# Kernel tuning notes

Hardware: AMD Instinct MI355X
Metric: run time of the kernel (lower is better)

Reference implementation:

```python
import jax, jax.numpy as jnp
import numpy as np

B, A, T, D, H, ATTN = 32, 128, 96, 16, 128, 64
MAX_DIST, EMB = 50, 32


def _ln(x, g, b, eps=1e-5):
    m = x.mean(-1, keepdims=True)
    v = ((x - m) ** 2).mean(-1, keepdims=True)
    return (x - m) / jnp.sqrt(v + eps) * g + b


def _lstm_layer(xs, Wih, Whh, bih, bhh):
    # xs: (N, T, Din); PyTorch gate order i, f, g, o
    n = xs.shape[0]
    h0 = jnp.zeros((n, Whh.shape[1]), xs.dtype)
    bias = bih + bhh
    def step(carry, x_t):
        h, c = carry
        gates = x_t @ Wih.T + h @ Whh.T + bias
        i, f, g, o = jnp.split(gates, 4, axis=-1)
        c = jax.nn.sigmoid(f) * c + jax.nn.sigmoid(i) * jnp.tanh(g)
        h = jax.nn.sigmoid(o) * jnp.tanh(c)
        return (h, c), h
    _, hs = jax.lax.scan(step, (h0, h0), jnp.swapaxes(xs, 0, 1))
    return jnp.swapaxes(hs, 0, 1)  # (N, T, H)


def _forward(ranks, x, W_ih0, W_hh0, b_ih0, b_hh0, W_ih1, W_hh1, b_ih1, b_hh1,
             attn_w, attn_W1, attn_W2, ln1_g, ln1_b, proj_W, proj_b,
             Wq, bq, Wk, bk, Wv, bv, rank_emb, rw1_W, rw1_b, rw2_W,
             ff1_W, ff1_b, ff2_W, ff2_b, ln2_g, ln2_b, sp1_W, sp1_b, sp2_W, sp2_b):
    b, a, t, d = x.shape
    xs = x.reshape(b * a, t, d)
    # LSTM-HA (dropout disabled, eval mode)
    h1 = _lstm_layer(xs, W_ih0, W_hh0, b_ih0, b_hh0)
    h2 = _lstm_layer(h1, W_ih1, W_hh1, b_ih1, b_hh1)
    hT = h2[:, -1, :]
    # additive history attention, vectorized over all timesteps
    alpha = jnp.tanh(h2 @ attn_W1 + (hT @ attn_W2)[:, None, :]) @ attn_w  # (b*a, t)
    w = jax.nn.softmax(alpha, axis=1)
    ctx = jnp.einsum('nt,nth->nh', w, h2)
    rep = _ln(ctx, ln1_g, ln1_b).reshape(b, a, -1)  # (b, a, H)
    # CAAN
    xp = rep @ proj_W + proj_b
    q = xp @ Wq + bq
    k = xp @ Wk + bk
    v = xp @ Wv + bv
    scores = jnp.einsum('bnd,bmd->bnm', q, k) / (ATTN ** 0.5)
    dist = jnp.clip(jnp.abs(ranks[:, :, None] - ranks[:, None, :]), 0, MAX_DIST)
    emb = rank_emb[dist]  # (b, a, a, EMB)
    gate = jax.nn.sigmoid(jax.nn.relu(emb @ rw1_W + rw1_b) @ rw2_W)  # (b, a, a)
    attn = jax.nn.softmax(scores * gate, axis=-1)
    ao = jnp.einsum('bnm,bmd->bnd', attn, v)
    ff = _ln(jax.nn.relu(ao @ ff1_W + ff1_b) @ ff2_W + ff2_b, ln2_g, ln2_b)
    return jax.nn.sigmoid((jax.nn.relu(ff @ sp1_W + sp1_b) @ sp2_W + sp2_b)[..., 0])


def setup_inputs() -> dict:
    key = jax.random.key(0)
    ks = jax.random.split(key, 40)
    it = iter(range(40))
    def rn(shape, s):
        return jax.random.normal(ks[next(it)], shape, jnp.float32) * s
    sH = 1.0 / float(np.sqrt(H))
    sA = 1.0 / float(np.sqrt(ATTN))
    return dict(
        x=jax.random.normal(ks[next(it)], (B, A, T, D), jnp.float32),
        ranks=jax.random.randint(ks[next(it)], (B, A), 0, A),
        W_ih0=rn((4 * H, D), sH), W_hh0=rn((4 * H, H), sH),
        b_ih0=jnp.zeros(4 * H), b_hh0=jnp.zeros(4 * H),
        W_ih1=rn((4 * H, H), sH), W_hh1=rn((4 * H, H), sH),
        b_ih1=jnp.zeros(4 * H), b_hh1=jnp.zeros(4 * H),
        attn_w=rn((H,), 0.06), attn_W1=rn((H, H), sH), attn_W2=rn((H, H), sH),
        ln1_g=jnp.ones(H), ln1_b=jnp.zeros(H),
        proj_W=rn((H, ATTN), sH), proj_b=jnp.zeros(ATTN),
        Wq=rn((ATTN, ATTN), sA), bq=jnp.zeros(ATTN),
        Wk=rn((ATTN, ATTN), sA), bk=jnp.zeros(ATTN),
        Wv=rn((ATTN, ATTN), sA), bv=jnp.zeros(ATTN),
        rank_emb=rn((MAX_DIST + 1, EMB), 1.0),
        rw1_W=rn((EMB, 16), 1.0 / float(np.sqrt(EMB))), rw1_b=jnp.zeros(16),
        rw2_W=rn((16,), 0.25),
        ff1_W=rn((ATTN, 2 * ATTN), sA), ff1_b=jnp.zeros(2 * ATTN),
        ff2_W=rn((2 * ATTN, ATTN), 1.0 / float(np.sqrt(2 * ATTN))), ff2_b=jnp.zeros(ATTN),
        ln2_g=jnp.ones(ATTN), ln2_b=jnp.zeros(ATTN),
        sp1_W=rn((ATTN, 32), sA), sp1_b=jnp.zeros(32),
        sp2_W=rn((32, 1), 0.18), sp2_b=jnp.zeros(1),
    )


def reference(x, ranks, W_ih0, W_hh0, b_ih0, b_hh0, W_ih1, W_hh1, b_ih1, b_hh1,
              attn_w, attn_W1, attn_W2, ln1_g, ln1_b, proj_W, proj_b,
              Wq, bq, Wk, bk, Wv, bv, rank_emb, rw1_W, rw1_b, rw2_W,
              ff1_W, ff1_b, ff2_W, ff2_b, ln2_g, ln2_b, sp1_W, sp1_b, sp2_W, sp2_b):
    return _forward(ranks, x, W_ih0, W_hh0, b_ih0, b_hh0, W_ih1, W_hh1, b_ih1, b_hh1,
                    attn_w, attn_W1, attn_W2, ln1_g, ln1_b, proj_W, proj_b,
                    Wq, bq, Wk, bk, Wv, bv, rank_emb, rw1_W, rw1_b, rw2_W,
                    ff1_W, ff1_b, ff2_W, ff2_b, ln2_g, ln2_b, sp1_W, sp1_b, sp2_W, sp2_b)
```

## Files before the change

### kernel.cpp

```cpp
#include <hip/hip_runtime.h>
#include <hip/hip_bf16.h>

namespace {

constexpr int T_ = 96;
constexpr int H_ = 128;

typedef short s8v __attribute__((ext_vector_type(8)));
typedef float f4v __attribute__((ext_vector_type(4)));

__device__ __forceinline__ float rcp_(float x) { return __builtin_amdgcn_rcpf(x); }
__device__ __forceinline__ float sig_(float x) { return rcp_(1.f + __expf(-x)); }
__device__ __forceinline__ float tanh_(float x) { return 1.f - 2.f * rcp_(__expf(2.f * x) + 1.f); }

__device__ __forceinline__ unsigned short bf16u(float f) {
  union { float f; unsigned u; } v; v.f = f;
  unsigned r = v.u + 0x7FFFu + ((v.u >> 16) & 1u);
  return (unsigned short)(r >> 16);
}
__device__ __forceinline__ float bf2f(unsigned short b) {
  union { unsigned u; float f; } v; v.u = ((unsigned)b) << 16;
  return v.f;
}

__device__ __forceinline__ s8v load8(const float* __restrict__ p) {
  const float4 a = *reinterpret_cast<const float4*>(p);
  const float4 b = *reinterpret_cast<const float4*>(p + 4);
  s8v r;
  r[0] = (short)bf16u(a.x); r[1] = (short)bf16u(a.y);
  r[2] = (short)bf16u(a.z); r[3] = (short)bf16u(a.w);
  r[4] = (short)bf16u(b.x); r[5] = (short)bf16u(b.y);
  r[6] = (short)bf16u(b.z); r[7] = (short)bf16u(b.w);
  return r;
}

__device__ __forceinline__ f4v mfma16(s8v a, s8v b, f4v c) {
  return __builtin_amdgcn_mfma_f32_16x16x32_bf16(a, b, c, 0, 0, 0);
}

__device__ __forceinline__ void barrier_lds() {
  __builtin_amdgcn_sched_barrier(0);
  asm volatile("s_waitcnt lgkmcnt(0)" ::: "memory");
  __builtin_amdgcn_s_barrier();
  __builtin_amdgcn_sched_barrier(0);
}

__global__ __launch_bounds__(64) void k0_gate(
    const float* __restrict__ remb,
    const float* __restrict__ rw1W, const float* __restrict__ rw1b,
    const float* __restrict__ rw2W,
    float* __restrict__ glut)
{
  const int d = threadIdx.x;
  if (d > 50) return;
  const float* er = remb + d * 32;
  float g = 0.f;
#pragma unroll
  for (int e = 0; e < 16; ++e) {
    float hs = rw1b[e];
#pragma unroll 8
    for (int i = 0; i < 32; ++i) hs += er[i] * rw1W[i * 16 + e];
    g += fmaxf(hs, 0.f) * rw2W[e];
  }
  glut[d] = sig_(g);
}

__global__ __launch_bounds__(256) void k0_w1(
    const float* __restrict__ W1, unsigned short* __restrict__ w1f)
{
  const int e = blockIdx.x * 256 + threadIdx.x;
  const int k = e >> 7, nn = e & 127;
  const int f = ((((nn >> 4) * 4 + (k >> 5)) * 4 + ((k >> 3) & 3)) * 16 + (nn & 15)) * 8 + (k & 7);
  w1f[f] = bf16u(W1[e]);
}

__global__ __launch_bounds__(256) void k0_whh1(
    const float* __restrict__ Whh1, unsigned short* __restrict__ whh1f)
{
  const int e = blockIdx.x * 256 + threadIdx.x;
  const int n = e >> 7, k = e & 127;
  const int g = n >> 7, wl = (n >> 4) & 7, l16 = n & 15;
  const int kt = k >> 5, lq = (k >> 3) & 3, i = k & 7;
  const int dst = (((g * 8 + wl) * 4 + kt) * 64 + lq * 16 + l16) * 8 + i;
  whh1f[dst] = bf16u(Whh1[e]);
}

__global__ __launch_bounds__(512) void k1_lstm_mfma(
    const float* __restrict__ x,
    const float* __restrict__ Wih0, const float* __restrict__ Whh0,
    const float* __restrict__ bih0, const float* __restrict__ bhh0,
    const float* __restrict__ Wih1, const float* __restrict__ whh1f,
    const float* __restrict__ bih1, const float* __restrict__ bhh1,
    unsigned short* __restrict__ hist)
{
  __shared__ __align__(16) unsigned short w1l[512 * 128];
  __shared__ __align__(16) unsigned short h1s[2][16 * 128];
  __shared__ __align__(16) unsigned short h2s[2][16 * 128];
  __shared__ __align__(16) unsigned short xb[2][16 * 32];

  const int tid  = threadIdx.x;
  const int lane = tid & 63;
  const int wv   = tid >> 6;
  const int l16  = lane & 15;
  const int lq   = lane >> 4;
  const int seqbase = blockIdx.x * 16;

  for (int i = tid; i < 2 * 16 * 128; i += 512) {
    (&h1s[0][0])[i] = 0; (&h2s[0][0])[i] = 0;
  }
  if (tid < 256) {
    const int s = tid >> 4, d = tid & 15;
    xb[0][s * 32 + 16 + d] = 0; xb[1][s * 32 + 16 + d] = 0;
    xb[0][s * 32 + d] = bf16u(x[((size_t)(seqbase + s) * T_ + 0) * 16 + d]);
  }
  {
    const uint4* src = reinterpret_cast<const uint4*>(whh1f);
    uint4* dst = reinterpret_cast<uint4*>(w1l);
    for (int i = tid; i < 8192; i += 512) dst[i] = src[i];
  }

  s8v whh0[4][4], wih1[4][4], wx0[4];
  float b0[4], b1[4];
  int wb[4];
#pragma unroll
  for (int g = 0; g < 4; ++g) {
    const int gr = g * 128 + 16 * wv + l16;
    b0[g] = bih0[gr] + bhh0[gr];
    b1[g] = bih1[gr] + bhh1[gr];
    wb[g] = ((g * 8 + wv) * 4) * 1024 + lane * 16;
#pragma unroll
    for (int kt = 0; kt < 4; ++kt) {
      const int k0 = kt * 32 + lq * 8;
      whh0[g][kt] = load8(Whh0 + (size_t)gr * 128 + k0);
      wih1[g][kt] = load8(Wih1 + (size_t)gr * 128 + k0);
    }
    if (lq < 2) wx0[g] = load8(Wih0 + (size_t)gr * 16 + lq * 8);
    else { s8v z; for (int i2 = 0; i2 < 8; ++i2) z[i2] = 0; wx0[g] = z; }
  }

  float c1[4] = {0.f, 0.f, 0.f, 0.f}, c2[4] = {0.f, 0.f, 0.f, 0.f};
  int cur = 0;
  __syncthreads();

  const int sw = (l16 & 7) << 4;
  const int hunit = 16 * wv + l16;

  for (int t = 0; t < T_; ++t) {
    const int xc = t & 1;
    float xv = 0.f;
    const bool xpf = (t + 1 < T_) && (tid < 256);
    if (xpf) {
      const int s = tid >> 4, d = tid & 15;
      xv = x[((size_t)(seqbase + s) * T_ + (t + 1)) * 16 + d];
    }

    f4v acc[4];
#pragma unroll
    for (int g = 0; g < 4; ++g) acc[g] = f4v{b0[g], b0[g], b0[g], b0[g]};
    {
      const s8v ax = *reinterpret_cast<const s8v*>(
          reinterpret_cast<const char*>(&xb[xc][0]) + l16 * 64 + lq * 16);
#pragma unroll
      for (int g = 0; g < 4; ++g) acc[g] = mfma16(ax, wx0[g], acc[g]);
    }
#pragma unroll
    for (int kt = 0; kt < 4; ++kt) {
      const s8v ah = *reinterpret_cast<const s8v*>(
          reinterpret_cast<const char*>(&h1s[cur][0]) + l16 * 256 +
          ((kt * 64 + lq * 16) ^ sw));
#pragma unroll
      for (int g = 0; g < 4; ++g) acc[g] = mfma16(ah, whh0[g][kt], acc[g]);
    }
#pragma unroll
    for (int ss = 0; ss < 4; ++ss) {
      const int seq = lq * 4 + ss;
      const float iv = sig_(acc[0][ss]);
      const float fv = sig_(acc[1][ss]);
      const float gv = tanh_(acc[2][ss]);
      const float ov = sig_(acc[3][ss]);
      c1[ss] = fv * c1[ss] + iv * gv;
      const float hv = ov * tanh_(c1[ss]);
      *reinterpret_cast<unsigned short*>(
          reinterpret_cast<char*>(&h1s[cur ^ 1][0]) + seq * 256 +
          ((2 * hunit) ^ ((seq & 7) << 4))) = bf16u(hv);
    }
    barrier_lds();

#pragma unroll
    for (int g = 0; g < 4; ++g) acc[g] = f4v{b1[g], b1[g], b1[g], b1[g]};
#pragma unroll
    for (int kt = 0; kt < 4; ++kt) {
      const int ko = (kt * 64 + lq * 16) ^ sw;
      const s8v a1 = *reinterpret_cast<const s8v*>(
          reinterpret_cast<const char*>(&h1s[cur ^ 1][0]) + l16 * 256 + ko);
      const s8v a2 = *reinterpret_cast<const s8v*>(
          reinterpret_cast<const char*>(&h2s[cur][0]) + l16 * 256 + ko);
#pragma unroll
      for (int g = 0; g < 4; ++g) {
        acc[g] = mfma16(a1, wih1[g][kt], acc[g]);
        const s8v bw = *reinterpret_cast<const s8v*>(
            reinterpret_cast<const char*>(w1l) + wb[g] + kt * 1024);
        acc[g] = mfma16(a2, bw, acc[g]);
      }
    }
#pragma unroll
    for (int ss = 0; ss < 4; ++ss) {
      const int seq = lq * 4 + ss;
      const float iv = sig_(acc[0][ss]);
      const float fv = sig_(acc[1][ss]);
      const float gv = tanh_(acc[2][ss]);
      const float ov = sig_(acc[3][ss]);
      c2[ss] = fv * c2[ss] + iv * gv;
      const float hv = ov * tanh_(c2[ss]);
      *reinterpret_cast<unsigned short*>(
          reinterpret_cast<char*>(&h2s[cur ^ 1][0]) + seq * 256 +
          ((2 * hunit) ^ ((seq & 7) << 4))) = bf16u(hv);
    }
    if (xpf) {
      const int s = tid >> 4, d = tid & 15;
      xb[xc ^ 1][s * 32 + d] = bf16u(xv);
    }
    barrier_lds();

    {
      const int seq = tid >> 5;
      const int u0  = (tid & 31) * 4;
      const uint2 v = *reinterpret_cast<const uint2*>(
          reinterpret_cast<const char*>(&h2s[cur ^ 1][0]) + seq * 256 +
          ((2 * u0) ^ ((seq & 7) << 4)));
      *reinterpret_cast<uint2*>(
          hist + ((size_t)(seqbase + seq) * T_ + t) * H_ + u0) = v;
    }
    cur ^= 1;
  }
}

__global__ __launch_bounds__(384, 2) void k2_pool_mfma(
    const unsigned short* __restrict__ hist,
    const unsigned short* __restrict__ w1f,
    const float* __restrict__ attn_w,
    const float* __restrict__ W2,
    const float* __restrict__ ln1g, const float* __restrict__ ln1b,
    float* __restrict__ rep)
{
  __shared__ __align__(16) unsigned short hst[96 * 128];
  __shared__ float sS[128], aws[128], alpha[96], wts[96], red[128], hTs[128];
  __shared__ float ctxP[3][128];

  const int n = blockIdx.x;
  const int tid = threadIdx.x;
  const int lane = tid & 63;
  const int wv = tid >> 6;
  const int l16 = lane & 15;
  const int lq = lane >> 4;

  const unsigned short* hsrc = hist + (size_t)n * T_ * H_;
  for (int i = tid; i < 1536; i += 384) {
    const int row = i >> 4, c16 = i & 15;
    const uint4 v = *reinterpret_cast<const uint4*>(hsrc + row * 128 + c16 * 8);
    *reinterpret_cast<uint4*>(
        reinterpret_cast<char*>(hst) + row * 256 + ((c16 * 16) ^ ((row & 7) << 4))) = v;
  }
  if (tid < 128) aws[tid] = attn_w[tid];
  __syncthreads();

  if (tid < 128) hTs[tid] = bf2f(hst[95 * 128 + (tid ^ 56)]);
  __syncthreads();
  if (tid < 128) {
    float s = 0.f;
    for (int h = 0; h < 128; ++h) s += hTs[h] * W2[(size_t)h * 128 + tid];
    sS[tid] = s;
  }
  __syncthreads();

  {
    const int row0 = wv * 16 + l16;
    f4v acc[8];
#pragma unroll
    for (int nt = 0; nt < 8; ++nt) acc[nt] = f4v{0.f, 0.f, 0.f, 0.f};
#pragma unroll
    for (int kt = 0; kt < 4; ++kt) {
      const s8v a = *reinterpret_cast<const s8v*>(
          reinterpret_cast<const char*>(hst) + row0 * 256 +
          ((kt * 64 + lq * 16) ^ ((row0 & 7) << 4)));
#pragma unroll
      for (int nt = 0; nt < 8; ++nt) {
        const s8v b = *reinterpret_cast<const s8v*>(
            w1f + ((((nt << 2) + kt) << 2 | lq) * 16 + l16) * 8);
        acc[nt] = mfma16(a, b, acc[nt]);
      }
    }
    float pa[4] = {0.f, 0.f, 0.f, 0.f};
#pragma unroll
    for (int nt = 0; nt < 8; ++nt) {
      const int col = nt * 16 + l16;
      const float ss = sS[col], aw = aws[col];
#pragma unroll
      for (int i2 = 0; i2 < 4; ++i2) pa[i2] += tanh_(acc[nt][i2] + ss) * aw;
    }
#pragma unroll
    for (int i2 = 0; i2 < 4; ++i2) {
      float v = pa[i2];
      v += __shfl_xor(v, 8); v += __shfl_xor(v, 4);
      v += __shfl_xor(v, 2); v += __shfl_xor(v, 1);
      if (l16 == 0) alpha[wv * 16 + lq * 4 + i2] = v;
    }
  }
  __syncthreads();

  if (tid < 128) red[tid] = (tid < 96) ? alpha[tid] : -1e30f;
  __syncthreads();
  for (int sft = 64; sft > 0; sft >>= 1) {
    if (tid < sft) red[tid] = fmaxf(red[tid], red[tid + sft]);
    __syncthreads();
  }
  const float mx = red[0];
  __syncthreads();
  if (tid < 128) {
    const float e = (tid < 96) ? __expf(alpha[tid] - mx) : 0.f;
    red[tid] = e;
    if (tid < 96) wts[tid] = e;
  }
  __syncthreads();
  for (int sft = 64; sft > 0; sft >>= 1) {
    if (tid < sft) red[tid] += red[tid + sft];
    __syncthreads();
  }
  const float inv = rcp_(red[0]);
  if (tid < 96) wts[tid] *= inv;
  __syncthreads();

  {
    const int th = tid >> 7, j = tid & 127;
    float cp = 0.f;
    for (int t = th * 32; t < th * 32 + 32; ++t)
      cp += wts[t] * bf2f(hst[t * 128 + (j ^ ((t & 7) << 3))]);
    ctxP[th][j] = cp;
  }
  __syncthreads();
  if (tid < 128) {
    hTs[tid] = ctxP[0][tid] + ctxP[1][tid] + ctxP[2][tid];
    red[tid] = hTs[tid];
  }
  __syncthreads();
  for (int sft = 64; sft > 0; sft >>= 1) {
    if (tid < sft) red[tid] += red[tid + sft];
    __syncthreads();
  }
  const float mean = red[0] * (1.f / 128.f);
  __syncthreads();
  if (tid < 128) { const float d = hTs[tid] - mean; red[tid] = d * d; }
  __syncthreads();
  for (int sft = 64; sft > 0; sft >>= 1) {
    if (tid < sft) red[tid] += red[tid + sft];
    __syncthreads();
  }
  const float var = red[0] * (1.f / 128.f);
  if (tid < 128)
    rep[(size_t)n * H_ + tid] =
        (hTs[tid] - mean) * rsqrtf(var + 1e-5f) * ln1g[tid] + ln1b[tid];
}

__global__ __launch_bounds__(256) void k3_qkv(
    const float* __restrict__ rep,
    const float* __restrict__ projW, const float* __restrict__ projb,
    const float* __restrict__ Wq, const float* __restrict__ bq,
    const float* __restrict__ Wk, const float* __restrict__ bk,
    const float* __restrict__ Wv, const float* __restrict__ bv,
    float* __restrict__ q, float* __restrict__ k, float* __restrict__ v)
{
  const int rbase = blockIdx.x * 32;
  const int tid = threadIdx.x;
  __shared__ float reps[32][128];
  __shared__ float xps[32][64];
  for (int i = tid; i < 32 * 128; i += 256)
    reps[i >> 7][i & 127] = rep[(size_t)(rbase + (i >> 7)) * 128 + (i & 127)];
  __syncthreads();
  const int col = tid & 63, rg = tid >> 6;
#pragma unroll 2
  for (int rr = 0; rr < 8; ++rr) {
    const int r = rg * 8 + rr;
    float acc = projb[col];
    for (int kk = 0; kk < 128; ++kk) acc += reps[r][kk] * projW[kk * 64 + col];
    xps[r][col] = acc;
  }
  __syncthreads();
#pragma unroll 2
  for (int rr = 0; rr < 8; ++rr) {
    const int r = rg * 8 + rr;
    float aq = bq[col], ak = bk[col], av = bv[col];
    for (int kk = 0; kk < 64; ++kk) {
      const float xv = xps[r][kk];
      aq += xv * Wq[kk * 64 + col];
      ak += xv * Wk[kk * 64 + col];
      av += xv * Wv[kk * 64 + col];
    }
    const size_t o = (size_t)(rbase + r) * 64 + col;
    q[o] = aq; k[o] = ak; v[o] = av;
  }
}

__global__ __launch_bounds__(512) void k4_attn_b(
    const float* __restrict__ q, const float* __restrict__ kbuf,
    const float* __restrict__ vbuf,
    const int* __restrict__ ranks, const float* __restrict__ glut,
    float* __restrict__ ao)
{
  __shared__ float Ks[128][65], Vs[128][65];
  __shared__ float qs[16][64];
  __shared__ float wrow[8][128];
  __shared__ float gl[51];
  __shared__ int rs[128];

  const int tid = threadIdx.x, lane = tid & 63, wv = tid >> 6;
  const int b = blockIdx.x >> 3;
  const int rowbase = (blockIdx.x & 7) * 16;

  for (int i = tid; i < 8192; i += 512) {
    Ks[i >> 6][i & 63] = kbuf[(size_t)b * 8192 + i];
    Vs[i >> 6][i & 63] = vbuf[(size_t)b * 8192 + i];
  }
  for (int i = tid; i < 1024; i += 512)
    qs[i >> 6][i & 63] = q[((size_t)b * 128 + rowbase) * 64 + i];
  if (tid < 128) rs[tid] = ranks[b * 128 + tid];
  if (tid >= 128 && tid < 179) gl[tid - 128] = glut[tid - 128];
  __syncthreads();

  const int m0 = lane, m1 = lane + 64;
#pragma unroll
  for (int rr = 0; rr < 2; ++rr) {
    const int lr = wv * 2 + rr;
    const int rn = rs[rowbase + lr];
    float s0 = 0.f, s1 = 0.f;
#pragma unroll 8
    for (int d = 0; d < 64; ++d) {
      const float qd = qs[lr][d];
      s0 += qd * Ks[m0][d];
      s1 += qd * Ks[m1][d];
    }
    int d0 = rn - rs[m0]; if (d0 < 0) d0 = -d0; if (d0 > 50) d0 = 50;
    int d1 = rn - rs[m1]; if (d1 < 0) d1 = -d1; if (d1 > 50) d1 = 50;
    s0 *= 0.125f * gl[d0];
    s1 *= 0.125f * gl[d1];
    float mx = fmaxf(s0, s1);
#pragma unroll
    for (int off = 32; off; off >>= 1) mx = fmaxf(mx, __shfl_xor(mx, off));
    const float e0 = __expf(s0 - mx), e1 = __expf(s1 - mx);
    float sum = e0 + e1;
#pragma unroll
    for (int off = 32; off; off >>= 1) sum += __shfl_xor(sum, off);
    const float inv = rcp_(sum);
    wrow[wv][m0] = e0 * inv;
    wrow[wv][m1] = e1 * inv;
    asm volatile("s_waitcnt lgkmcnt(0)" ::: "memory");
    float acc = 0.f;
#pragma unroll 4
    for (int m = 0; m < 128; ++m) acc += wrow[wv][m] * Vs[m][lane];
    ao[((size_t)b * 128 + rowbase + lr) * 64 + lane] = acc;
  }
}

__global__ __launch_bounds__(128) void k5_ffout(
    const float* __restrict__ ao,
    const float* __restrict__ ff1W, const float* __restrict__ ff1b,
    const float* __restrict__ ff2W, const float* __restrict__ ff2b,
    const float* __restrict__ ln2g, const float* __restrict__ ln2b,
    const float* __restrict__ sp1W, const float* __restrict__ sp1b,
    const float* __restrict__ sp2W, const float* __restrict__ sp2b,
    float* __restrict__ out)
{
  const int row = blockIdx.x;
  const int tid = threadIdx.x;
  __shared__ float aos[64], hid[128], ffs[64], red[128], h2b[32];
  if (tid < 64) aos[tid] = ao[(size_t)row * 64 + tid];
  __syncthreads();
  float hv = ff1b[tid];
  for (int dd = 0; dd < 64; ++dd) hv += aos[dd] * ff1W[dd * 128 + tid];
  hid[tid] = fmaxf(hv, 0.f);
  __syncthreads();
  float yv = 0.f;
  if (tid < 64) {
    yv = ff2b[tid];
    for (int h2 = 0; h2 < 128; ++h2) yv += hid[h2] * ff2W[h2 * 64 + tid];
  }
  red[tid] = (tid < 64) ? yv : 0.f;
  __syncthreads();
  for (int sft = 64; sft > 0; sft >>= 1) {
    if (tid < sft) red[tid] += red[tid + sft];
    __syncthreads();
  }
  const float mean = red[0] * (1.f / 64.f);
  __syncthreads();
  {
    const float d2 = (tid < 64) ? (yv - mean) : 0.f;
    red[tid] = d2 * d2;
  }
  __syncthreads();
  for (int sft = 64; sft > 0; sft >>= 1) {
    if (tid < sft) red[tid] += red[tid + sft];
    __syncthreads();
  }
  const float var = red[0] * (1.f / 64.f);
  __syncthreads();
  if (tid < 64) ffs[tid] = (yv - mean) * rsqrtf(var + 1e-5f) * ln2g[tid] + ln2b[tid];
  __syncthreads();
  if (tid < 32) {
    float h2v = sp1b[tid];
    for (int c = 0; c < 64; ++c) h2v += ffs[c] * sp1W[c * 32 + tid];
    h2b[tid] = fmaxf(h2v, 0.f);
  }
  __syncthreads();
  if (tid == 0) {
    float o = sp2b[0];
#pragma unroll
    for (int e2 = 0; e2 < 32; ++e2) o += h2b[e2] * sp2W[e2];
    out[row] = sig_(o);
  }
}

}

extern "C" void kernel_launch(void* const* d_in, const int* in_sizes, int n_in,
                              void* d_out, int out_size, void* d_ws, size_t ws_size,
                              hipStream_t stream)
{
  const float* x      = (const float*)d_in[0];
  const int*   ranks  = (const int*)  d_in[1];
  const float* Wih0   = (const float*)d_in[2];
  const float* Whh0   = (const float*)d_in[3];
  const float* bih0   = (const float*)d_in[4];
  const float* bhh0   = (const float*)d_in[5];
  const float* Wih1   = (const float*)d_in[6];
  const float* Whh1   = (const float*)d_in[7];
  const float* bih1   = (const float*)d_in[8];
  const float* bhh1   = (const float*)d_in[9];
  const float* attn_w = (const float*)d_in[10];
  const float* W1     = (const float*)d_in[11];
  const float* W2     = (const float*)d_in[12];
  const float* ln1g   = (const float*)d_in[13];
  const float* ln1b   = (const float*)d_in[14];
  const float* projW  = (const float*)d_in[15];
  const float* projb  = (const float*)d_in[16];
  const float* Wq     = (const float*)d_in[17];
  const float* bq     = (const float*)d_in[18];
  const float* Wk     = (const float*)d_in[19];
  const float* bk     = (const float*)d_in[20];
  const float* Wv     = (const float*)d_in[21];
  const float* bv     = (const float*)d_in[22];
  const float* remb   = (const float*)d_in[23];
  const float* rw1W   = (const float*)d_in[24];
  const float* rw1b   = (const float*)d_in[25];
  const float* rw2W   = (const float*)d_in[26];
  const float* ff1W   = (const float*)d_in[27];
  const float* ff1b   = (const float*)d_in[28];
  const float* ff2W   = (const float*)d_in[29];
  const float* ff2b   = (const float*)d_in[30];
  const float* ln2g   = (const float*)d_in[31];
  const float* ln2b   = (const float*)d_in[32];
  const float* sp1W   = (const float*)d_in[33];
  const float* sp1b   = (const float*)d_in[34];
  const float* sp2W   = (const float*)d_in[35];
  const float* sp2b   = (const float*)d_in[36];
  float* out = (float*)d_out;

  char* ws = (char*)d_ws;
  unsigned short* hist = (unsigned short*)ws;
  size_t off = (size_t)4096 * 96 * 128 * 2;
  float* rep = (float*)(ws + off); off += (size_t)4096 * 128 * 4;
  float* qb  = (float*)(ws + off); off += (size_t)4096 * 64 * 4;
  float* kb  = (float*)(ws + off); off += (size_t)4096 * 64 * 4;
  float* vb  = (float*)(ws + off); off += (size_t)4096 * 64 * 4;
  float* aob = (float*)(ws + off); off += (size_t)4096 * 64 * 4;
  unsigned short* w1f   = (unsigned short*)(ws + off); off += 16384 * 2;
  float* glut = (float*)(ws + off); off += 64 * 4;
  unsigned short* whh1f = (unsigned short*)(ws + off); off += 65536 * 2;

  k0_gate<<<dim3(1), dim3(64), 0, stream>>>(remb, rw1W, rw1b, rw2W, glut);
  k0_w1<<<dim3(64), dim3(256), 0, stream>>>(W1, w1f);
  k0_whh1<<<dim3(256), dim3(256), 0, stream>>>(Whh1, whh1f);
  k1_lstm_mfma<<<dim3(256), dim3(512), 0, stream>>>(
      x, Wih0, Whh0, bih0, bhh0, Wih1, (const float*)whh1f, bih1, bhh1, hist);
  k2_pool_mfma<<<dim3(4096), dim3(384), 0, stream>>>(
      hist, w1f, attn_w, W2, ln1g, ln1b, rep);
  k3_qkv<<<dim3(128), dim3(256), 0, stream>>>(
      rep, projW, projb, Wq, bq, Wk, bk, Wv, bv, qb, kb, vb);
  k4_attn_b<<<dim3(256), dim3(512), 0, stream>>>(
      qb, kb, vb, ranks, glut, aob);
  k5_ffout<<<dim3(4096), dim3(128), 0, stream>>>(
      aob, ff1W, ff1b, ff2W, ff2b, ln2g, ln2b, sp1W, sp1b, sp2W, sp2b, out);
}
```

Before: 399.0 us.

## Fuse projection and QKV into pooling kernel; batch FF head per wave

The projection and Q/K/V matmuls move into the tail of the pooling kernel, so each sequence block computes them from its layer-normed context and the separate QKV kernel plus the rep round-trip go away. The FF/output head kernel is rewritten so each 512-thread block stages all FF weights in shared memory once and processes 8 rows, one per wave, with shuffle-based reductions in place of shared-memory tree reductions. This removes a launch, reduces redundant global weight reads and barrier counts, but lengthens the pooling kernel with serial small matmuls that use only part of its threads.

```diff
diff --git a/kernel.cpp b/kernel.cpp
--- a/kernel.cpp
+++ b/kernel.cpp
@@ -241,11 +241,16 @@
     const float* __restrict__ attn_w,
     const float* __restrict__ W2,
     const float* __restrict__ ln1g, const float* __restrict__ ln1b,
-    float* __restrict__ rep)
+    const float* __restrict__ projW, const float* __restrict__ projb,
+    const float* __restrict__ Wq, const float* __restrict__ bq,
+    const float* __restrict__ Wk, const float* __restrict__ bk,
+    const float* __restrict__ Wv, const float* __restrict__ bv,
+    float* __restrict__ qb_, float* __restrict__ kb_, float* __restrict__ vb_)
 {
   __shared__ __align__(16) unsigned short hst[96 * 128];
   __shared__ float sS[128], aws[128], alpha[96], wts[96], red[128], hTs[128];
   __shared__ float ctxP[3][128];
+  __shared__ float xps[64];
 
   const int n = blockIdx.x;
   const int tid = threadIdx.x;
@@ -356,47 +361,24 @@
     __syncthreads();
   }
   const float var = red[0] * (1.f / 128.f);
+  __syncthreads();
   if (tid < 128)
-    rep[(size_t)n * H_ + tid] =
-        (hTs[tid] - mean) * rsqrtf(var + 1e-5f) * ln1g[tid] + ln1b[tid];
-}
-
-__global__ __launch_bounds__(256) void k3_qkv(
-    const float* __restrict__ rep,
-    const float* __restrict__ projW, const float* __restrict__ projb,
-    const float* __restrict__ Wq, const float* __restrict__ bq,
-    const float* __restrict__ Wk, const float* __restrict__ bk,
-    const float* __restrict__ Wv, const float* __restrict__ bv,
-    float* __restrict__ q, float* __restrict__ k, float* __restrict__ v)
-{
-  const int rbase = blockIdx.x * 32;
-  const int tid = threadIdx.x;
-  __shared__ float reps[32][128];
-  __shared__ float xps[32][64];
-  for (int i = tid; i < 32 * 128; i += 256)
-    reps[i >> 7][i & 127] = rep[(size_t)(rbase + (i >> 7)) * 128 + (i & 127)];
-  __syncthreads();
-  const int col = tid & 63, rg = tid >> 6;
-#pragma unroll 2
-  for (int rr = 0; rr < 8; ++rr) {
-    const int r = rg * 8 + rr;
-    float acc = projb[col];
-    for (int kk = 0; kk < 128; ++kk) acc += reps[r][kk] * projW[kk * 64 + col];
-    xps[r][col] = acc;
-  }
-  __syncthreads();
-#pragma unroll 2
-  for (int rr = 0; rr < 8; ++rr) {
-    const int r = rg * 8 + rr;
-    float aq = bq[col], ak = bk[col], av = bv[col];
-    for (int kk = 0; kk < 64; ++kk) {
-      const float xv = xps[r][kk];
-      aq += xv * Wq[kk * 64 + col];
-      ak += xv * Wk[kk * 64 + col];
-      av += xv * Wv[kk * 64 + col];
-    }
-    const size_t o = (size_t)(rbase + r) * 64 + col;
-    q[o] = aq; k[o] = ak; v[o] = av;
+    hTs[tid] = (hTs[tid] - mean) * rsqrtf(var + 1e-5f) * ln1g[tid] + ln1b[tid];
+  __syncthreads();
+  if (tid < 64) {
+    float xpv = projb[tid];
+    for (int kk = 0; kk < 128; ++kk) xpv += hTs[kk] * projW[kk * 64 + tid];
+    xps[tid] = xpv;
+  }
+  __syncthreads();
+  if (tid < 192) {
+    const int which = tid >> 6, col = tid & 63;
+    const float* W = (which == 0) ? Wq : (which == 1) ? Wk : Wv;
+    const float* bb = (which == 0) ? bq : (which == 1) ? bk : bv;
+    float acc = bb[col];
+    for (int kk = 0; kk < 64; ++kk) acc += xps[kk] * W[kk * 64 + col];
+    float* dst = (which == 0) ? qb_ : (which == 1) ? kb_ : vb_;
+    dst[(size_t)n * 64 + col] = acc;
   }
 }
 
@@ -460,7 +442,7 @@
   }
 }
 
-__global__ __launch_bounds__(128) void k5_ffout(
+__global__ __launch_bounds__(512) void k5_ffout_w(
     const float* __restrict__ ao,
     const float* __restrict__ ff1W, const float* __restrict__ ff1b,
     const float* __restrict__ ff2W, const float* __restrict__ ff2b,
@@ -469,53 +451,61 @@
     const float* __restrict__ sp2W, const float* __restrict__ sp2b,
     float* __restrict__ out)
 {
-  const int row = blockIdx.x;
-  const int tid = threadIdx.x;
-  __shared__ float aos[64], hid[128], ffs[64], red[128], h2b[32];
-  if (tid < 64) aos[tid] = ao[(size_t)row * 64 + tid];
-  __syncthreads();
-  float hv = ff1b[tid];
-  for (int dd = 0; dd < 64; ++dd) hv += aos[dd] * ff1W[dd * 128 + tid];
-  hid[tid] = fmaxf(hv, 0.f);
-  __syncthreads();
-  float yv = 0.f;
-  if (tid < 64) {
-    yv = ff2b[tid];
-    for (int h2 = 0; h2 < 128; ++h2) yv += hid[h2] * ff2W[h2 * 64 + tid];
-  }
-  red[tid] = (tid < 64) ? yv : 0.f;
-  __syncthreads();
-  for (int sft = 64; sft > 0; sft >>= 1) {
-    if (tid < sft) red[tid] += red[tid + sft];
-    __syncthreads();
-  }
-  const float mean = red[0] * (1.f / 64.f);
-  __syncthreads();
-  {
-    const float d2 = (tid < 64) ? (yv - mean) : 0.f;
-    red[tid] = d2 * d2;
-  }
-  __syncthreads();
-  for (int sft = 64; sft > 0; sft >>= 1) {
-    if (tid < sft) red[tid] += red[tid + sft];
-    __syncthreads();
-  }
-  const float var = red[0] * (1.f / 64.f);
-  __syncthreads();
-  if (tid < 64) ffs[tid] = (yv - mean) * rsqrtf(var + 1e-5f) * ln2g[tid] + ln2b[tid];
-  __syncthreads();
-  if (tid < 32) {
-    float h2v = sp1b[tid];
-    for (int c = 0; c < 64; ++c) h2v += ffs[c] * sp1W[c * 32 + tid];
-    h2b[tid] = fmaxf(h2v, 0.f);
-  }
-  __syncthreads();
-  if (tid == 0) {
-    float o = sp2b[0];
-#pragma unroll
-    for (int e2 = 0; e2 < 32; ++e2) o += h2b[e2] * sp2W[e2];
-    out[row] = sig_(o);
-  }
+  __shared__ float f1[64][128];
+  __shared__ float f2[128][64];
+  __shared__ float s1[64][32];
+  __shared__ float f1b[128], f2b[64], g2[64], b2[64], s1b[32], s2w[32];
+  __shared__ float hbuf[8][128], fbuf[8][64];
+
+  const int tid = threadIdx.x, lane = tid & 63, wv = tid >> 6;
+  for (int i = tid; i < 8192; i += 512) f1[i >> 7][i & 127] = ff1W[i];
+  for (int i = tid; i < 8192; i += 512) f2[i >> 6][i & 63] = ff2W[i];
+  for (int i = tid; i < 2048; i += 512) s1[i >> 5][i & 31] = sp1W[i];
+  if (tid < 128) f1b[tid] = ff1b[tid];
+  else if (tid < 192) f2b[tid - 128] = ff2b[tid - 128];
+  else if (tid < 256) g2[tid - 192] = ln2g[tid - 192];
+  else if (tid < 320) b2[tid - 256] = ln2b[tid - 256];
+  else if (tid < 352) s1b[tid - 320] = sp1b[tid - 320];
+  else if (tid < 384) s2w[tid - 352] = sp2W[tid - 352];
+  __syncthreads();
+
+  const int row = blockIdx.x * 8 + wv;
+  const float a = ao[(size_t)row * 64 + lane];
+  float h0 = f1b[lane], h1 = f1b[lane + 64];
+#pragma unroll 8
+  for (int d = 0; d < 64; ++d) {
+    const float ad = __shfl(a, d);
+    h0 += ad * f1[d][lane];
+    h1 += ad * f1[d][lane + 64];
+  }
+  hbuf[wv][lane] = fmaxf(h0, 0.f);
+  hbuf[wv][lane + 64] = fmaxf(h1, 0.f);
+  __syncthreads();
+
+  float yv = f2b[lane];
+#pragma unroll 8
+  for (int j = 0; j < 128; ++j) yv += hbuf[wv][j] * f2[j][lane];
+  float s = yv;
+#pragma unroll
+  for (int off = 32; off; off >>= 1) s += __shfl_xor(s, off);
+  const float mean = s * (1.f / 64.f);
+  float d2 = (yv - mean) * (yv - mean);
+#pragma unroll
+  for (int off = 32; off; off >>= 1) d2 += __shfl_xor(d2, off);
+  const float var = d2 * (1.f / 64.f);
+  fbuf[wv][lane] = (yv - mean) * rsqrtf(var + 1e-5f) * g2[lane] + b2[lane];
+  __syncthreads();
+
+  float val = 0.f;
+  if (lane < 32) {
+    float h2v = s1b[lane];
+#pragma unroll 8
+    for (int c = 0; c < 64; ++c) h2v += fbuf[wv][c] * s1[c][lane];
+    val = fmaxf(h2v, 0.f) * s2w[lane];
+  }
+#pragma unroll
+  for (int off = 16; off; off >>= 1) val += __shfl_xor(val, off);
+  if (lane == 0) out[row] = sig_(val + sp2b[0]);
 }
 
 }
@@ -574,6 +564,7 @@
   unsigned short* w1f   = (unsigned short*)(ws + off); off += 16384 * 2;
   float* glut = (float*)(ws + off); off += 64 * 4;
   unsigned short* whh1f = (unsigned short*)(ws + off); off += 65536 * 2;
+  (void)rep;
 
   k0_gate<<<dim3(1), dim3(64), 0, stream>>>(remb, rw1W, rw1b, rw2W, glut);
   k0_w1<<<dim3(64), dim3(256), 0, stream>>>(W1, w1f);
@@ -581,11 +572,10 @@
   k1_lstm_mfma<<<dim3(256), dim3(512), 0, stream>>>(
       x, Wih0, Whh0, bih0, bhh0, Wih1, (const float*)whh1f, bih1, bhh1, hist);
   k2_pool_mfma<<<dim3(4096), dim3(384), 0, stream>>>(
-      hist, w1f, attn_w, W2, ln1g, ln1b, rep);
-  k3_qkv<<<dim3(128), dim3(256), 0, stream>>>(
-      rep, projW, projb, Wq, bq, Wk, bk, Wv, bv, qb, kb, vb);
+      hist, w1f, attn_w, W2, ln1g, ln1b,
+      projW, projb, Wq, bq, Wk, bk, Wv, bv, qb, kb, vb);
   k4_attn_b<<<dim3(256), dim3(512), 0, stream>>>(
       qb, kb, vb, ranks, glut, aob);
-  k5_ffout<<<dim3(4096), dim3(128), 0, stream>>>(
+  k5_ffout_w<<<dim3(512), dim3(512), 0, stream>>>(
       aob, ff1W, ff1b, ff2W, ff2b, ln2g, ln2b, sp1W, sp1b, sp2W, sp2b, out);
 }
```

New measurement: 393.9 us, median of 2. About the same (-1.3%).
